# Performance work log

Hardware: AMD Instinct MI355X
Metric: run time of the kernel (lower is better)

The kernel has to match this reference:

```python
import jax, jax.numpy as jnp
import numpy as np

B, N_BOX, NUM_CLASSES = 32, 50, 20
FEATURE_SIZES = np.array([[52, 52], [26, 26], [13, 13]])
NUM_CENG = FEATURE_SIZES[:, 0] * FEATURE_SIZES[:, 1]            # [2704, 676, 169]
NUM_TOTAL = int((NUM_CENG * 3).sum())                            # 10647
ANCS_SCALE = np.array([[10, 13], [16, 30], [33, 23], [30, 61], [62, 45],
                       [59, 119], [116, 90], [156, 198], [373, 326]], dtype=np.float32) / 416.0
NEG_IOU_THRESHOLD = 0.5
NUM_NEG = 1000
EPS = 1e-7

def _build_anchor_grid():
    # rows ordered: level(52,26,13) -> cell (row-major) -> 3 anchors per cell
    out = []
    for lvl in range(3):
        f = int(FEATURE_SIZES[lvl, 0])
        ys, xs = np.meshgrid(np.arange(f), np.arange(f), indexing='ij')
        xy = (np.stack([xs, ys], -1).reshape(-1, 2).astype(np.float32)) / f  # cell corner (col/f,row/f)
        xy3 = np.repeat(xy, 3, axis=0)                                       # [f*f*3, 2]
        wh3 = np.tile(ANCS_SCALE[lvl * 3:(lvl + 1) * 3], (f * f, 1))
        out.append(np.concatenate([xy3, wh3], 1))
    return np.concatenate(out, 0)                                            # [10647, 4]

ANCS = jnp.asarray(_build_anchor_grid())
FSIZES = jnp.asarray(np.repeat(FEATURE_SIZES[:, 0].astype(np.float32), NUM_CENG * 3))  # [10647]
OFF_CENG = jnp.asarray([0.0, 2704.0, 3380.0])   # prefix sums of NUM_CENG
FW_LVL = jnp.asarray([52.0, 26.0, 13.0])


def _xywh2ltrb(xywh):
    return jnp.concatenate([xywh[..., :2] - xywh[..., 2:] * 0.5,
                            xywh[..., :2] + xywh[..., 2:] * 0.5], -1)


def _ciou(a, b):
    # a, b: broadcastable [..., 4] ltrb -> CIoU [...]
    lt = jnp.maximum(a[..., :2], b[..., :2])
    rb = jnp.minimum(a[..., 2:], b[..., 2:])
    wh = jnp.clip(rb - lt, 0.0)
    inter = wh[..., 0] * wh[..., 1]
    wa = a[..., 2] - a[..., 0]; ha = a[..., 3] - a[..., 1]
    wb = b[..., 2] - b[..., 0]; hb = b[..., 3] - b[..., 1]
    union = wa * ha + wb * hb - inter
    iou = inter / (union + EPS)
    clt = jnp.minimum(a[..., :2], b[..., :2])
    crb = jnp.maximum(a[..., 2:], b[..., 2:])
    cwh = crb - clt
    c2 = cwh[..., 0] ** 2 + cwh[..., 1] ** 2 + EPS
    ctr_a = (a[..., :2] + a[..., 2:]) * 0.5
    ctr_b = (b[..., :2] + b[..., 2:]) * 0.5
    rho2 = jnp.sum((ctr_a - ctr_b) ** 2, -1)
    v = (4.0 / (jnp.pi ** 2)) * (jnp.arctan(wa / (ha + EPS)) - jnp.arctan(wb / (hb + EPS))) ** 2
    alpha = jax.lax.stop_gradient(v / (1.0 - iou + v + EPS))
    return iou - rho2 / c2 - alpha * v


def _bce(p, t):
    p = jnp.clip(p, EPS, 1.0 - EPS)
    return -(t * jnp.log(p) + (1.0 - t) * jnp.log(1.0 - p))


def _per_image(p, boxes, labels):
    # p: [10647, 25], boxes: [N,4] ltrb, labels: [N] (1-based)
    N = boxes.shape[0]
    bxy = (boxes[:, :2] + boxes[:, 2:]) * 0.5
    bwh = boxes[:, 2:] - boxes[:, :2]
    # ---- anchor-target matching (source's loop always takes argmax anchor) ----
    p1xy = jnp.repeat(bxy, 9, axis=0)                                       # [N*9, 2]
    fpairs = jnp.repeat(jnp.asarray(FEATURE_SIZES, jnp.float32), 3, axis=0)  # [9, 2]
    p2f = jnp.tile(fpairs, (N, 1))                                          # [N*9, 2]
    colrow = jnp.floor(p1xy * p2f)                                          # (col, row) per box/anchor
    anc_xy = colrow / p2f
    anc_wh = jnp.tile(jnp.asarray(ANCS_SCALE), (N, 1))
    anc_ltrb = _xywh2ltrb(jnp.concatenate([anc_xy, anc_wh], 1))
    ids = jnp.arange(N, dtype=boxes.dtype)
    iou_m = _ciou(boxes[:, None, :] + ids[:, None, None],
                  anc_ltrb[None, :, :] + jnp.repeat(ids, 9)[None, :, None])  # [N, N*9]
    k = jnp.argmax(iou_m, axis=1) % 9                                       # best anchor id 0..8
    lvl = k // 3                                                            # (source quirk: //len(NUMS_ANC))
    cr = colrow[jnp.arange(N) * 9 + k]                                      # [N, 2]
    off_cr = cr[:, 1] * FW_LVL[lvl] + cr[:, 0]
    midx = ((OFF_CENG[lvl] + off_cr) * 3.0 + lvl.astype(jnp.float32)).astype(jnp.int32)  # [N]
    # ---- decode predictions ----
    p_box_xy = p[:, :2] / FSIZES[:, None] + ANCS[:, :2]
    p_box_wh = jnp.exp(p[:, 2:4]) * ANCS[:, 2:]
    p_ltrb = _xywh2ltrb(jnp.concatenate([p_box_xy, p_box_wh], -1))          # [10647, 4]
    # ---- positive losses ----
    pcls = p[midx, 5:]                                                      # [N, C]
    t = jax.nn.one_hot(labels - 1, NUM_CLASSES, dtype=pcls.dtype)
    l_cls = _bce(pcls, t).sum()
    pconf = p[midx, 4]
    l_conf_p = (-jnp.log(jnp.clip(pconf, EPS, 1.0 - EPS))).sum()
    ciou_pos = _ciou(boxes, p_ltrb[midx])                                   # [N]
    w = 2.0 - bwh[:, 0] * bwh[:, 1]
    l_box = (w * (1.0 - ciou_pos)).sum()
    # ---- negative conf loss (replicates filtered-coordinate indexing) ----
    iou_all = _ciou(boxes[:, None, :], p_ltrb[None, :, :])                  # [N, 10647]
    mx = iou_all.max(axis=0)
    mask = mx < NEG_IOU_THRESHOLD
    key = jnp.where(mask, mx, jnp.inf)
    order = jnp.argsort(key)                                                # masked-in first, ascending
    rank = jnp.cumsum(mask) - 1                                             # filtered coordinate per row
    neg_idx = rank[order][:NUM_NEG]                                         # == source's _max_index[:NUM_NEG]
    pneg = p[neg_idx, 4]
    l_conf_n = (-jnp.log(jnp.clip(1.0 - pneg, EPS, 1.0 - EPS))).sum()
    nf = jnp.asarray(N, p.dtype)
    return l_cls / nf, l_box / nf, l_conf_p / nf, l_conf_n


def setup_inputs() -> dict:
    key = jax.random.key(0)
    k1, k2, k3, k4 = jax.random.split(key, 4)
    p_yolo_ts = jax.random.uniform(k1, (B, NUM_TOTAL, 4 + 1 + NUM_CLASSES),
                                   dtype=jnp.float32, minval=1e-4, maxval=1.0 - 1e-4)
    cxy = jax.random.uniform(k2, (B, N_BOX, 2), minval=0.15, maxval=0.85)
    wh = jax.random.uniform(k3, (B, N_BOX, 2), minval=0.05, maxval=0.25)
    boxes = jnp.concatenate([cxy - wh * 0.5, cxy + wh * 0.5], -1).astype(jnp.float32)
    labels = jax.random.randint(k4, (B, N_BOX), 1, NUM_CLASSES + 1, dtype=jnp.int32)
    return {"p_yolo_ts": p_yolo_ts, "boxes": boxes, "labels": labels}


def reference(p_yolo_ts, boxes, labels):
    l_cls, l_box, l_cp, l_cn = jax.vmap(_per_image)(p_yolo_ts, boxes, labels)
    return l_cp.mean() + l_cn.mean() + l_box.mean() + l_cls.mean()
```

## Files before the change

kernel.cpp:

```cpp
#include <hip/hip_runtime.h>

namespace {

constexpr int BB   = 32;
constexpr int NBOX = 50;
constexpr int NCLS = 20;
constexpr int NT   = 10647;
constexpr int NNEG = 1000;
constexpr int DEC_BLOCKS = (NT + 127) / 128;
constexpr int POS_BLOCKS = (NBOX + 3) / 4;
constexpr float EPS = 1e-7f;
constexpr float PI4 = (float)(4.0 / 9.869604401089358);

__device__ __constant__ float c_aw[9] = {10.f/416.f,16.f/416.f,33.f/416.f,30.f/416.f,62.f/416.f,59.f/416.f,116.f/416.f,156.f/416.f,373.f/416.f};
__device__ __constant__ float c_ah[9] = {13.f/416.f,30.f/416.f,23.f/416.f,61.f/416.f,45.f/416.f,119.f/416.f,90.f/416.f,198.f/416.f,326.f/416.f};

__device__ __forceinline__ float fastrcp(float x) {
  return __builtin_amdgcn_rcpf(x);
}

__device__ __forceinline__ float dciou(float al, float at, float ar, float ab,
                                       float bl, float bt, float br, float bb,
                                       float atanA, float atanB) {
  float ltx = fmaxf(al, bl), lty = fmaxf(at, bt);
  float rbx = fminf(ar, br), rby = fminf(ab, bb);
  float wx = fmaxf(rbx - ltx, 0.f), wy = fmaxf(rby - lty, 0.f);
  float inter = wx * wy;
  float wa = ar - al, ha = ab - at;
  float wb = br - bl, hb = bb - bt;
  float uni = wa * ha + wb * hb - inter;
  float iou = inter / (uni + EPS);
  float cw = fmaxf(ar, br) - fminf(al, bl);
  float ch = fmaxf(ab, bb) - fminf(at, bt);
  float c2 = cw * cw + ch * ch + EPS;
  float dx = (al + ar) * 0.5f - (bl + br) * 0.5f;
  float dy = (at + ab) * 0.5f - (bt + bb) * 0.5f;
  float rho2 = dx * dx + dy * dy;
  float dat = atanA - atanB;
  float v = PI4 * (dat * dat);
  float alpha = v / (1.f - iou + v + EPS);
  return iou - rho2 / c2 - alpha * v;
}

__device__ __forceinline__ int wave_incl_scan(int x, int lane) {
  #pragma unroll
  for (int off = 1; off < 64; off <<= 1) {
    int y = __shfl_up(x, off);
    if (lane >= off) x += y;
  }
  return x;
}

__global__ __launch_bounds__(256) void k_main(const float* __restrict__ p,
                            const float* __restrict__ boxes,
                            const int* __restrict__ labels,
                            unsigned long long* __restrict__ comp,
                            float* __restrict__ pcls, float* __restrict__ pbox,
                            float* __restrict__ pcp, float* __restrict__ out) {
  const int b = blockIdx.y;
  const int tid = threadIdx.x;
  if (blockIdx.x == 0 && b == 0 && tid == 0) out[0] = 0.f;

  if (blockIdx.x < DEC_BLOCKS) {
    __shared__ float4 sA[NBOX];
    __shared__ float4 sE[NBOX];
    if (tid < NBOX) {
      const float* bp = boxes + (b * NBOX + tid) * 4;
      float l = bp[0], t = bp[1], r = bp[2], d = bp[3];
      sA[tid] = make_float4(l, t, r, d);
      float wa = r - l, ha = d - t;
      sE[tid] = make_float4((l + r) * 0.5f, (t + d) * 0.5f,
                            atanf(wa / (ha + EPS)), wa * ha);
    }
    __syncthreads();

    const int par = tid & 1;
    const int j = blockIdx.x * 128 + (tid >> 1);
    if (j >= NT) return;

    int lvl = (j < 8112) ? 0 : ((j < 10140) ? 1 : 2);
    int jb0 = (lvl == 0) ? 0 : ((lvl == 1) ? 8112 : 10140);
    int f   = (lvl == 0) ? 52 : ((lvl == 1) ? 26 : 13);
    int jj = j - jb0;
    int cell = jj / 3, a = jj % 3 + lvl * 3;
    int x = cell % f, y = cell / f;
    float ff = (float)f;
    const float* pr = p + ((size_t)b * NT + j) * 25;
    float px = pr[0] / ff + (float)x / ff;
    float py = pr[1] / ff + (float)y / ff;
    float pw = expf(pr[2]) * c_aw[a];
    float ph = expf(pr[3]) * c_ah[a];
    float bl = px - pw * 0.5f, bt = py - ph * 0.5f;
    float br = px + pw * 0.5f, bbv = py + ph * 0.5f;
    float wb = br - bl, hb = bbv - bt;
    float areab = wb * hb;
    float cxb = (bl + br) * 0.5f, cyb = (bt + bbv) * 0.5f;
    float atb = atanf(wb / (hb + EPS));

    float mx = -INFINITY;
    for (int i = par; i < NBOX; i += 2) {
      float4 A = sA[i];
      float ltx = fmaxf(A.x, bl), lty = fmaxf(A.y, bt);
      float rbx = fminf(A.z, br), rby = fminf(A.w, bbv);
      float wx = fmaxf(rbx - ltx, 0.f), wy = fmaxf(rby - lty, 0.f);
      float inter = wx * wy;
      bool need = (inter > 0.f) || (mx < 0.f);
      if (__any(need)) {
        float4 E = sE[i];
        float uni = E.w + areab - inter;
        float iou = inter * fastrcp(uni + EPS);
        float cw = fmaxf(A.z, br) - fminf(A.x, bl);
        float ch = fmaxf(A.w, bbv) - fminf(A.y, bt);
        float c2 = cw * cw + ch * ch + EPS;
        float dx = E.x - cxb;
        float dy = E.y - cyb;
        float rho2 = dx * dx + dy * dy;
        float dat = E.z - atb;
        float v = PI4 * (dat * dat);
        float alpha = v * fastrcp(1.f - iou + v + EPS);
        float ci = iou - rho2 * fastrcp(c2) - alpha * v;
        mx = fmaxf(mx, ci);
      }
    }
    mx = fmaxf(mx, __shfl_xor(mx, 1));

    if (par == 0) {
      float key = (mx < 0.5f) ? mx : INFINITY;
      unsigned int u = __float_as_uint(key);
      u = (u & 0x80000000u) ? ~u : (u | 0x80000000u);
      comp[(size_t)b * NT + j] = ((unsigned long long)u << 14) | (unsigned long long)j;
    }
  } else {
    const int lane = tid & 63;
    const int wave = tid >> 6;
    const int i = (blockIdx.x - DEC_BLOCKS) * 4 + wave;

    __shared__ float scx[NBOX], scy[NBOX];
    if (tid < NBOX) {
      const float* bp = boxes + (b * NBOX + tid) * 4;
      float l = bp[0], t = bp[1], r = bp[2], d = bp[3];
      scx[tid] = (l + r) * 0.5f;
      scy[tid] = (t + d) * 0.5f;
    }
    __syncthreads();
    if (i >= NBOX) return;

    const float* bi = boxes + (b * NBOX + i) * 4;
    float bl0 = bi[0], bt0 = bi[1], br0 = bi[2], bd0 = bi[3];
    float fi = (float)i;
    float al = bl0 + fi, at = bt0 + fi, ar = br0 + fi, ad = bd0 + fi;
    float wa = ar - al, ha = ad - at;
    float atanA = atanf(wa / (ha + EPS));

    float bestv = -INFINITY; int bestm = 1 << 30;
    #pragma unroll
    for (int m = lane; m < 9 * NBOX; m += 64) {
      int jb = m / 9, aa = m % 9;
      float fa = (aa < 3) ? 52.f : (aa < 6 ? 26.f : 13.f);
      float col = floorf(scx[jb] * fa);
      float row = floorf(scy[jb] * fa);
      float ax = col / fa, ay = row / fa;
      float aw = c_aw[aa], ah = c_ah[aa];
      float fj = (float)jb;
      float bl = (ax - aw * 0.5f) + fj;
      float bt = (ay - ah * 0.5f) + fj;
      float br = (ax + aw * 0.5f) + fj;
      float bd = (ay + ah * 0.5f) + fj;
      float wb = br - bl, hb = bd - bt;
      float atanB = atanf(wb / (hb + EPS));
      float v = dciou(al, at, ar, ad, bl, bt, br, bd, atanA, atanB);
      if (v > bestv) { bestv = v; bestm = m; }
    }
    #pragma unroll
    for (int off = 32; off > 0; off >>= 1) {
      float ov = __shfl_down(bestv, off);
      int om = __shfl_down(bestm, off);
      if (ov > bestv || (ov == bestv && om < bestm)) { bestv = ov; bestm = om; }
    }
    int bm = __shfl(bestm, 0);

    int k = bm % 9;
    int lvl = k / 3;
    float fk = (k < 3) ? 52.f : (k < 6 ? 26.f : 13.f);
    float col = floorf(scx[i] * fk);
    float row = floorf(scy[i] * fk);
    float offc = (lvl == 0) ? 0.f : (lvl == 1 ? 2704.f : 3380.f);
    int midx = (int)((offc + row * fk + col) * 3.0f + (float)lvl);

    const float* prm = p + ((size_t)b * NT + midx) * 25;
    int lab = labels[b * NBOX + i] - 1;

    float lc = 0.f;
    if (lane < NCLS) {
      float pc = prm[5 + lane];
      pc = fminf(fmaxf(pc, EPS), 1.f - EPS);
      float tt = (lane == lab) ? 1.f : 0.f;
      lc = -(tt * logf(pc) + (1.f - tt) * logf(1.f - pc));
    }
    #pragma unroll
    for (int off = 32; off > 0; off >>= 1) lc += __shfl_down(lc, off);

    if (lane == 0) {
      pcls[b * NBOX + i] = lc;
      float pc4 = prm[4];
      pc4 = fminf(fmaxf(pc4, EPS), 1.f - EPS);
      pcp[b * NBOX + i] = -logf(pc4);

      int lvl2 = (midx < 8112) ? 0 : ((midx < 10140) ? 1 : 2);
      int jb0 = (lvl2 == 0) ? 0 : ((lvl2 == 1) ? 8112 : 10140);
      int f2  = (lvl2 == 0) ? 52 : ((lvl2 == 1) ? 26 : 13);
      int jj2 = midx - jb0;
      int cell2 = jj2 / 3, a2 = jj2 % 3 + lvl2 * 3;
      int xx = cell2 % f2, yy = cell2 / f2;
      float ff2 = (float)f2;
      float px = prm[0] / ff2 + (float)xx / ff2;
      float py = prm[1] / ff2 + (float)yy / ff2;
      float pw = expf(prm[2]) * c_aw[a2];
      float ph = expf(prm[3]) * c_ah[a2];
      float pbl = px - pw * 0.5f, pbt = py - ph * 0.5f;
      float pbr = px + pw * 0.5f, pbd = py + ph * 0.5f;

      float wb = pbr - pbl, hb = pbd - pbt;
      float atanB = atanf(wb / (hb + EPS));
      float wa0 = br0 - bl0, ha0 = bd0 - bt0;
      float atanA0 = atanf(wa0 / (ha0 + EPS));
      float cp = dciou(bl0, bt0, br0, bd0, pbl, pbt, pbr, pbd, atanA0, atanB);
      float w = 2.f - wa0 * ha0;
      pbox[b * NBOX + i] = w * (1.f - cp);
    }
  }
}

__global__ __launch_bounds__(1024) void k_neg2(const unsigned long long* __restrict__ comp,
                                               const float* __restrict__ p,
                                               const float* __restrict__ pcls,
                                               const float* __restrict__ pbox,
                                               const float* __restrict__ pcp,
                                               float* __restrict__ out) {
  int b = blockIdx.x;
  const unsigned long long* c = comp + (size_t)b * NT;
  const int tid = threadIdx.x, lane = tid & 63, wave = tid >> 6;

  __shared__ int hist[4096];
  __shared__ int s_w[16];
  __shared__ unsigned long long s_pref;
  __shared__ int s_rem;
  __shared__ int s_digit;
  __shared__ int s_rem_next;
  __shared__ int s_cnt;
  __shared__ float s_facc[16];
  __shared__ float s_lcn;
  __shared__ int s_tot[11][16];
  __shared__ int s_off[11][16];

  unsigned long long v[11];
  #pragma unroll
  for (int k = 0; k < 11; ++k) {
    int j = k * 1024 + tid;
    v[k] = (j < NT) ? c[j] : ~0ull;
  }

  int wincl[11];
  #pragma unroll
  for (int k = 0; k < 11; ++k) {
    unsigned long long x = v[k];
    int flag = ((x >> 14) < 0xFF800000ull) ? 1 : 0;
    int incl = wave_incl_scan(flag, lane);
    wincl[k] = incl;
    if (lane == 63) s_tot[k][wave] = incl;
  }
  __syncthreads();
  if (wave == 0) {
    int i0 = lane * 3;
    int a0 = (i0     < 176) ? s_tot[i0 / 16][i0 % 16] : 0;
    int a1 = (i0 + 1 < 176) ? s_tot[(i0 + 1) / 16][(i0 + 1) % 16] : 0;
    int a2 = (i0 + 2 < 176) ? s_tot[(i0 + 2) / 16][(i0 + 2) % 16] : 0;
    int lsum = a0 + a1 + a2;
    int linc = wave_incl_scan(lsum, lane);
    int lexc = linc - lsum;
    if (i0     < 176) s_off[i0 / 16][i0 % 16] = lexc;
    if (i0 + 1 < 176) s_off[(i0 + 1) / 16][(i0 + 1) % 16] = lexc + a0;
    if (i0 + 2 < 176) s_off[(i0 + 2) / 16][(i0 + 2) % 16] = lexc + a0 + a1;
    if (lane == 63) s_cnt = linc;
  }
  if (tid == 0) { s_pref = 0ull; s_rem = NNEG - 1; }
  __syncthreads();
  const bool spec = (s_cnt >= NNEG);

  for (int pass = 0; pass < 4; ++pass) {
    int lo = 36 - pass * 12;
    for (int h = tid; h < 4096; h += 1024) hist[h] = 0;
    __syncthreads();
    unsigned long long pref = s_pref;
    #pragma unroll
    for (int k = 0; k < 11; ++k) {
      unsigned long long x = v[k];
      bool fin = ((x >> 14) < 0xFF800000ull);
      if ((!spec || fin) && (x >> (lo + 12)) == (pref >> (lo + 12)))
        atomicAdd(&hist[(int)((x >> lo) & 4095ull)], 1);
    }
    __syncthreads();
    int base = tid * 4;
    int c0 = hist[base], c1 = hist[base + 1], c2 = hist[base + 2], c3 = hist[base + 3];
    int tsum = c0 + c1 + c2 + c3;
    int incl = wave_incl_scan(tsum, lane);
    if (lane == 63) s_w[wave] = incl;
    __syncthreads();
    if (wave == 0) {
      int wv = (lane < 16) ? s_w[lane] : 0;
      int wincl2 = wave_incl_scan(wv, lane);
      if (lane < 16) s_w[lane] = wincl2 - wv;
    }
    __syncthreads();
    int excl = incl - tsum + s_w[wave];
    int rem = s_rem;
    int p0 = excl, p1 = p0 + c0, p2 = p1 + c1, p3 = p2 + c2;
    if (rem >= p0 && rem < p0 + c0) { s_digit = base + 0; s_rem_next = rem - p0; }
    if (rem >= p1 && rem < p1 + c1) { s_digit = base + 1; s_rem_next = rem - p1; }
    if (rem >= p2 && rem < p2 + c2) { s_digit = base + 2; s_rem_next = rem - p2; }
    if (rem >= p3 && rem < p3 + c3) { s_digit = base + 3; s_rem_next = rem - p3; }
    __syncthreads();
    if (tid == 0) {
      s_pref |= ((unsigned long long)s_digit) << lo;
      s_rem = s_rem_next;
    }
    __syncthreads();
  }
  const unsigned long long T = s_pref;

  float acc = 0.f;
  const float* pb = p + (size_t)b * NT * 25;
  #pragma unroll
  for (int k = 0; k < 11; ++k) {
    unsigned long long x = v[k];
    if (x <= T) {
      int idx = s_off[k][wave] + wincl[k] - 1;
      if (idx < 0) idx += NT;
      float q = 1.f - pb[(size_t)idx * 25 + 4];
      q = fminf(fmaxf(q, EPS), 1.f - EPS);
      acc += -logf(q);
    }
  }

  #pragma unroll
  for (int off = 32; off > 0; off >>= 1) acc += __shfl_down(acc, off);
  if (lane == 0) s_facc[wave] = acc;
  __syncthreads();
  if (tid == 0) {
    float s = 0.f;
    #pragma unroll
    for (int w = 0; w < 16; ++w) s += s_facc[w];
    s_lcn = s;
  }
  __syncthreads();

  if (wave == 0) {
    float s3 = 0.f;
    if (lane < NBOX)
      s3 = pcls[b * NBOX + lane] + pbox[b * NBOX + lane] + pcp[b * NBOX + lane];
    #pragma unroll
    for (int off = 32; off > 0; off >>= 1) s3 += __shfl_down(s3, off);
    if (lane == 0)
      atomicAdd(out, (s3 / (float)NBOX + s_lcn) / (float)BB);
  }
}

}

extern "C" void kernel_launch(void* const* d_in, const int* in_sizes, int n_in,
                              void* d_out, int out_size, void* d_ws, size_t ws_size,
                              hipStream_t stream) {
  const float* p      = (const float*)d_in[0];
  const float* boxes  = (const float*)d_in[1];
  const int*   labels = (const int*)d_in[2];
  float* out = (float*)d_out;

  char* ws = (char*)d_ws;
  size_t off = 0;
  unsigned long long* comp = (unsigned long long*)(ws + off); off += (size_t)BB * NT * sizeof(unsigned long long);
  float* pcls = (float*)(ws + off);                off += BB * NBOX * sizeof(float);
  float* pbox = (float*)(ws + off);                off += BB * NBOX * sizeof(float);
  float* pcp  = (float*)(ws + off);                off += BB * NBOX * sizeof(float);

  dim3 g1(DEC_BLOCKS + POS_BLOCKS, BB);
  k_main<<<g1, 256, 0, stream>>>(p, boxes, labels, comp, pcls, pbox, pcp, out);
  k_neg2<<<BB, 1024, 0, stream>>>(comp, p, pcls, pbox, pcp, out);
}
```

Before: 56.79 us.

## Fuse decode, positive and negative-selection kernels into one with per-image counters

```diff
diff --git a/kernel.cpp b/kernel.cpp
--- a/kernel.cpp
+++ b/kernel.cpp
@@ -7,8 +7,9 @@
 constexpr int NCLS = 20;
 constexpr int NT   = 10647;
 constexpr int NNEG = 1000;
-constexpr int DEC_BLOCKS = (NT + 127) / 128;
-constexpr int POS_BLOCKS = (NBOX + 3) / 4;
+constexpr int DECB = (NT + 511) / 512;
+constexpr int POSB = (NBOX + 15) / 16;
+constexpr int NPUB = DECB + POSB;
 constexpr float EPS = 1e-7f;
 constexpr float PI4 = (float)(4.0 / 9.869604401089358);
 
@@ -51,17 +52,18 @@
   return x;
 }
 
-__global__ __launch_bounds__(256) void k_main(const float* __restrict__ p,
+__global__ __launch_bounds__(1024) void k_all(const float* __restrict__ p,
                             const float* __restrict__ boxes,
                             const int* __restrict__ labels,
                             unsigned long long* __restrict__ comp,
                             float* __restrict__ pcls, float* __restrict__ pbox,
-                            float* __restrict__ pcp, float* __restrict__ out) {
+                            float* __restrict__ pcp, int* __restrict__ ctr,
+                            float* __restrict__ out) {
   const int b = blockIdx.y;
   const int tid = threadIdx.x;
-  if (blockIdx.x == 0 && b == 0 && tid == 0) out[0] = 0.f;
-
-  if (blockIdx.x < DEC_BLOCKS) {
+  const int lane = tid & 63, wave = tid >> 6;
+
+  if (blockIdx.x < DECB) {
     __shared__ float4 sA[NBOX];
     __shared__ float4 sE[NBOX];
     if (tid < NBOX) {
@@ -75,38 +77,36 @@
     __syncthreads();
 
     const int par = tid & 1;
-    const int j = blockIdx.x * 128 + (tid >> 1);
-    if (j >= NT) return;
-
-    int lvl = (j < 8112) ? 0 : ((j < 10140) ? 1 : 2);
-    int jb0 = (lvl == 0) ? 0 : ((lvl == 1) ? 8112 : 10140);
-    int f   = (lvl == 0) ? 52 : ((lvl == 1) ? 26 : 13);
-    int jj = j - jb0;
-    int cell = jj / 3, a = jj % 3 + lvl * 3;
-    int x = cell % f, y = cell / f;
-    float ff = (float)f;
-    const float* pr = p + ((size_t)b * NT + j) * 25;
-    float px = pr[0] / ff + (float)x / ff;
-    float py = pr[1] / ff + (float)y / ff;
-    float pw = expf(pr[2]) * c_aw[a];
-    float ph = expf(pr[3]) * c_ah[a];
-    float bl = px - pw * 0.5f, bt = py - ph * 0.5f;
-    float br = px + pw * 0.5f, bbv = py + ph * 0.5f;
-    float wb = br - bl, hb = bbv - bt;
-    float areab = wb * hb;
-    float cxb = (bl + br) * 0.5f, cyb = (bt + bbv) * 0.5f;
-    float atb = atanf(wb / (hb + EPS));
-
-    float mx = -INFINITY;
-    for (int i = par; i < NBOX; i += 2) {
-      float4 A = sA[i];
-      float ltx = fmaxf(A.x, bl), lty = fmaxf(A.y, bt);
-      float rbx = fminf(A.z, br), rby = fminf(A.w, bbv);
-      float wx = fmaxf(rbx - ltx, 0.f), wy = fmaxf(rby - lty, 0.f);
-      float inter = wx * wy;
-      bool need = (inter > 0.f) || (mx < 0.f);
-      if (__any(need)) {
+    const int j = blockIdx.x * 512 + (tid >> 1);
+    if (j < NT) {
+      int lvl = (j < 8112) ? 0 : ((j < 10140) ? 1 : 2);
+      int jb0 = (lvl == 0) ? 0 : ((lvl == 1) ? 8112 : 10140);
+      int f   = (lvl == 0) ? 52 : ((lvl == 1) ? 26 : 13);
+      int jj = j - jb0;
+      int cell = jj / 3, a = jj % 3 + lvl * 3;
+      int x = cell % f, y = cell / f;
+      float ff = (float)f;
+      const float* pr = p + ((size_t)b * NT + j) * 25;
+      float px = pr[0] / ff + (float)x / ff;
+      float py = pr[1] / ff + (float)y / ff;
+      float pw = expf(pr[2]) * c_aw[a];
+      float ph = expf(pr[3]) * c_ah[a];
+      float bl = px - pw * 0.5f, bt = py - ph * 0.5f;
+      float br = px + pw * 0.5f, bbv = py + ph * 0.5f;
+      float wb = br - bl, hb = bbv - bt;
+      float areab = wb * hb;
+      float cxb = (bl + br) * 0.5f, cyb = (bt + bbv) * 0.5f;
+      float atb = atanf(wb / (hb + EPS));
+
+      float mx = -INFINITY;
+      #pragma unroll 5
+      for (int i = par; i < NBOX; i += 2) {
+        float4 A = sA[i];
         float4 E = sE[i];
+        float ltx = fmaxf(A.x, bl), lty = fmaxf(A.y, bt);
+        float rbx = fminf(A.z, br), rby = fminf(A.w, bbv);
+        float wx = fmaxf(rbx - ltx, 0.f), wy = fmaxf(rby - lty, 0.f);
+        float inter = wx * wy;
         float uni = E.w + areab - inter;
         float iou = inter * fastrcp(uni + EPS);
         float cw = fmaxf(A.z, br) - fminf(A.x, bl);
@@ -121,19 +121,20 @@
         float ci = iou - rho2 * fastrcp(c2) - alpha * v;
         mx = fmaxf(mx, ci);
       }
-    }
-    mx = fmaxf(mx, __shfl_xor(mx, 1));
-
-    if (par == 0) {
-      float key = (mx < 0.5f) ? mx : INFINITY;
-      unsigned int u = __float_as_uint(key);
-      u = (u & 0x80000000u) ? ~u : (u | 0x80000000u);
-      comp[(size_t)b * NT + j] = ((unsigned long long)u << 14) | (unsigned long long)j;
-    }
-  } else {
-    const int lane = tid & 63;
-    const int wave = tid >> 6;
-    const int i = (blockIdx.x - DEC_BLOCKS) * 4 + wave;
+      mx = fmaxf(mx, __shfl_xor(mx, 1));
+
+      if (par == 0) {
+        float key = (mx < 0.5f) ? mx : INFINITY;
+        unsigned int u = __float_as_uint(key);
+        u = (u & 0x80000000u) ? ~u : (u | 0x80000000u);
+        comp[(size_t)b * NT + j] = ((unsigned long long)u << 14) | (unsigned long long)j;
+      }
+    }
+    __syncthreads();
+    if (tid == 0) { __threadfence(); atomicAdd(&ctr[b], 1); }
+
+  } else if (blockIdx.x < NPUB) {
+    const int i = (blockIdx.x - DECB) * 16 + wave;
 
     __shared__ float scx[NBOX], scy[NBOX];
     if (tid < NBOX) {
@@ -143,225 +144,225 @@
       scy[tid] = (t + d) * 0.5f;
     }
     __syncthreads();
-    if (i >= NBOX) return;
-
-    const float* bi = boxes + (b * NBOX + i) * 4;
-    float bl0 = bi[0], bt0 = bi[1], br0 = bi[2], bd0 = bi[3];
-    float fi = (float)i;
-    float al = bl0 + fi, at = bt0 + fi, ar = br0 + fi, ad = bd0 + fi;
-    float wa = ar - al, ha = ad - at;
-    float atanA = atanf(wa / (ha + EPS));
-
-    float bestv = -INFINITY; int bestm = 1 << 30;
+
+    if (i < NBOX) {
+      const float* bi = boxes + (b * NBOX + i) * 4;
+      float bl0 = bi[0], bt0 = bi[1], br0 = bi[2], bd0 = bi[3];
+      float fi = (float)i;
+      float al = bl0 + fi, at = bt0 + fi, ar = br0 + fi, ad = bd0 + fi;
+      float wa = ar - al, ha = ad - at;
+      float atanA = atanf(wa / (ha + EPS));
+
+      float bestv = -INFINITY; int bestm = 1 << 30;
+      #pragma unroll
+      for (int m = lane; m < 9 * NBOX; m += 64) {
+        int jb = m / 9, aa = m % 9;
+        float fa = (aa < 3) ? 52.f : (aa < 6 ? 26.f : 13.f);
+        float col = floorf(scx[jb] * fa);
+        float row = floorf(scy[jb] * fa);
+        float ax = col / fa, ay = row / fa;
+        float aw = c_aw[aa], ah = c_ah[aa];
+        float fj = (float)jb;
+        float bl = (ax - aw * 0.5f) + fj;
+        float bt = (ay - ah * 0.5f) + fj;
+        float br = (ax + aw * 0.5f) + fj;
+        float bd = (ay + ah * 0.5f) + fj;
+        float wb = br - bl, hb = bd - bt;
+        float atanB = atanf(wb / (hb + EPS));
+        float v = dciou(al, at, ar, ad, bl, bt, br, bd, atanA, atanB);
+        if (v > bestv) { bestv = v; bestm = m; }
+      }
+      #pragma unroll
+      for (int off = 32; off > 0; off >>= 1) {
+        float ov = __shfl_down(bestv, off);
+        int om = __shfl_down(bestm, off);
+        if (ov > bestv || (ov == bestv && om < bestm)) { bestv = ov; bestm = om; }
+      }
+      int bm = __shfl(bestm, 0);
+
+      int k = bm % 9;
+      int lvl = k / 3;
+      float fk = (k < 3) ? 52.f : (k < 6 ? 26.f : 13.f);
+      float col = floorf(scx[i] * fk);
+      float row = floorf(scy[i] * fk);
+      float offc = (lvl == 0) ? 0.f : (lvl == 1 ? 2704.f : 3380.f);
+      int midx = (int)((offc + row * fk + col) * 3.0f + (float)lvl);
+
+      const float* prm = p + ((size_t)b * NT + midx) * 25;
+      int lab = labels[b * NBOX + i] - 1;
+
+      float lc = 0.f;
+      if (lane < NCLS) {
+        float pc = prm[5 + lane];
+        pc = fminf(fmaxf(pc, EPS), 1.f - EPS);
+        float tt = (lane == lab) ? 1.f : 0.f;
+        lc = -(tt * logf(pc) + (1.f - tt) * logf(1.f - pc));
+      }
+      #pragma unroll
+      for (int off = 32; off > 0; off >>= 1) lc += __shfl_down(lc, off);
+
+      if (lane == 0) {
+        pcls[b * NBOX + i] = lc;
+        float pc4 = prm[4];
+        pc4 = fminf(fmaxf(pc4, EPS), 1.f - EPS);
+        pcp[b * NBOX + i] = -logf(pc4);
+
+        int lvl2 = (midx < 8112) ? 0 : ((midx < 10140) ? 1 : 2);
+        int jb0 = (lvl2 == 0) ? 0 : ((lvl2 == 1) ? 8112 : 10140);
+        int f2  = (lvl2 == 0) ? 52 : ((lvl2 == 1) ? 26 : 13);
+        int jj2 = midx - jb0;
+        int cell2 = jj2 / 3, a2 = jj2 % 3 + lvl2 * 3;
+        int xx = cell2 % f2, yy = cell2 / f2;
+        float ff2 = (float)f2;
+        float px = prm[0] / ff2 + (float)xx / ff2;
+        float py = prm[1] / ff2 + (float)yy / ff2;
+        float pw = expf(prm[2]) * c_aw[a2];
+        float ph = expf(prm[3]) * c_ah[a2];
+        float pbl = px - pw * 0.5f, pbt = py - ph * 0.5f;
+        float pbr = px + pw * 0.5f, pbd = py + ph * 0.5f;
+
+        float wb = pbr - pbl, hb = pbd - pbt;
+        float atanB = atanf(wb / (hb + EPS));
+        float wa0 = br0 - bl0, ha0 = bd0 - bt0;
+        float atanA0 = atanf(wa0 / (ha0 + EPS));
+        float cp = dciou(bl0, bt0, br0, bd0, pbl, pbt, pbr, pbd, atanA0, atanB);
+        float w = 2.f - wa0 * ha0;
+        pbox[b * NBOX + i] = w * (1.f - cp);
+      }
+    }
+    __syncthreads();
+    if (tid == 0) { __threadfence(); atomicAdd(&ctr[b], 1); }
+
+  } else {
+    if (tid == 0) {
+      while (atomicAdd(&ctr[b], 0) < NPUB) __builtin_amdgcn_s_sleep(2);
+      __threadfence();
+    }
+    __syncthreads();
+
+    const unsigned long long* c = comp + (size_t)b * NT;
+    __shared__ int hist[4096];
+    __shared__ int s_w[16];
+    __shared__ unsigned long long s_pref;
+    __shared__ int s_rem;
+    __shared__ int s_digit;
+    __shared__ int s_rem_next;
+    __shared__ int s_cnt;
+    __shared__ float s_facc[16];
+    __shared__ float s_lcn;
+    __shared__ int s_tot[11][16];
+    __shared__ int s_off[11][16];
+
+    unsigned long long v[11];
     #pragma unroll
-    for (int m = lane; m < 9 * NBOX; m += 64) {
-      int jb = m / 9, aa = m % 9;
-      float fa = (aa < 3) ? 52.f : (aa < 6 ? 26.f : 13.f);
-      float col = floorf(scx[jb] * fa);
-      float row = floorf(scy[jb] * fa);
-      float ax = col / fa, ay = row / fa;
-      float aw = c_aw[aa], ah = c_ah[aa];
-      float fj = (float)jb;
-      float bl = (ax - aw * 0.5f) + fj;
-      float bt = (ay - ah * 0.5f) + fj;
-      float br = (ax + aw * 0.5f) + fj;
-      float bd = (ay + ah * 0.5f) + fj;
-      float wb = br - bl, hb = bd - bt;
-      float atanB = atanf(wb / (hb + EPS));
-      float v = dciou(al, at, ar, ad, bl, bt, br, bd, atanA, atanB);
-      if (v > bestv) { bestv = v; bestm = m; }
-    }
-    #pragma unroll
-    for (int off = 32; off > 0; off >>= 1) {
-      float ov = __shfl_down(bestv, off);
-      int om = __shfl_down(bestm, off);
-      if (ov > bestv || (ov == bestv && om < bestm)) { bestv = ov; bestm = om; }
-    }
-    int bm = __shfl(bestm, 0);
-
-    int k = bm % 9;
-    int lvl = k / 3;
-    float fk = (k < 3) ? 52.f : (k < 6 ? 26.f : 13.f);
-    float col = floorf(scx[i] * fk);
-    float row = floorf(scy[i] * fk);
-    float offc = (lvl == 0) ? 0.f : (lvl == 1 ? 2704.f : 3380.f);
-    int midx = (int)((offc + row * fk + col) * 3.0f + (float)lvl);
-
-    const float* prm = p + ((size_t)b * NT + midx) * 25;
-    int lab = labels[b * NBOX + i] - 1;
-
-    float lc = 0.f;
-    if (lane < NCLS) {
-      float pc = prm[5 + lane];
-      pc = fminf(fmaxf(pc, EPS), 1.f - EPS);
-      float tt = (lane == lab) ? 1.f : 0.f;
-      lc = -(tt * logf(pc) + (1.f - tt) * logf(1.f - pc));
-    }
-    #pragma unroll
-    for (int off = 32; off > 0; off >>= 1) lc += __shfl_down(lc, off);
-
-    if (lane == 0) {
-      pcls[b * NBOX + i] = lc;
-      float pc4 = prm[4];
-      pc4 = fminf(fmaxf(pc4, EPS), 1.f - EPS);
-      pcp[b * NBOX + i] = -logf(pc4);
-
-      int lvl2 = (midx < 8112) ? 0 : ((midx < 10140) ? 1 : 2);
-      int jb0 = (lvl2 == 0) ? 0 : ((lvl2 == 1) ? 8112 : 10140);
-      int f2  = (lvl2 == 0) ? 52 : ((lvl2 == 1) ? 26 : 13);
-      int jj2 = midx - jb0;
-      int cell2 = jj2 / 3, a2 = jj2 % 3 + lvl2 * 3;
-      int xx = cell2 % f2, yy = cell2 / f2;
-      float ff2 = (float)f2;
-      float px = prm[0] / ff2 + (float)xx / ff2;
-      float py = prm[1] / ff2 + (float)yy / ff2;
-      float pw = expf(prm[2]) * c_aw[a2];
-      float ph = expf(prm[3]) * c_ah[a2];
-      float pbl = px - pw * 0.5f, pbt = py - ph * 0.5f;
-      float pbr = px + pw * 0.5f, pbd = py + ph * 0.5f;
-
-      float wb = pbr - pbl, hb = pbd - pbt;
-      float atanB = atanf(wb / (hb + EPS));
-      float wa0 = br0 - bl0, ha0 = bd0 - bt0;
-      float atanA0 = atanf(wa0 / (ha0 + EPS));
-      float cp = dciou(bl0, bt0, br0, bd0, pbl, pbt, pbr, pbd, atanA0, atanB);
-      float w = 2.f - wa0 * ha0;
-      pbox[b * NBOX + i] = w * (1.f - cp);
-    }
-  }
-}
-
-__global__ __launch_bounds__(1024) void k_neg2(const unsigned long long* __restrict__ comp,
-                                               const float* __restrict__ p,
-                                               const float* __restrict__ pcls,
-                                               const float* __restrict__ pbox,
-                                               const float* __restrict__ pcp,
-                                               float* __restrict__ out) {
-  int b = blockIdx.x;
-  const unsigned long long* c = comp + (size_t)b * NT;
-  const int tid = threadIdx.x, lane = tid & 63, wave = tid >> 6;
-
-  __shared__ int hist[4096];
-  __shared__ int s_w[16];
-  __shared__ unsigned long long s_pref;
-  __shared__ int s_rem;
-  __shared__ int s_digit;
-  __shared__ int s_rem_next;
-  __shared__ int s_cnt;
-  __shared__ float s_facc[16];
-  __shared__ float s_lcn;
-  __shared__ int s_tot[11][16];
-  __shared__ int s_off[11][16];
-
-  unsigned long long v[11];
-  #pragma unroll
-  for (int k = 0; k < 11; ++k) {
-    int j = k * 1024 + tid;
-    v[k] = (j < NT) ? c[j] : ~0ull;
-  }
-
-  int wincl[11];
-  #pragma unroll
-  for (int k = 0; k < 11; ++k) {
-    unsigned long long x = v[k];
-    int flag = ((x >> 14) < 0xFF800000ull) ? 1 : 0;
-    int incl = wave_incl_scan(flag, lane);
-    wincl[k] = incl;
-    if (lane == 63) s_tot[k][wave] = incl;
-  }
-  __syncthreads();
-  if (wave == 0) {
-    int i0 = lane * 3;
-    int a0 = (i0     < 176) ? s_tot[i0 / 16][i0 % 16] : 0;
-    int a1 = (i0 + 1 < 176) ? s_tot[(i0 + 1) / 16][(i0 + 1) % 16] : 0;
-    int a2 = (i0 + 2 < 176) ? s_tot[(i0 + 2) / 16][(i0 + 2) % 16] : 0;
-    int lsum = a0 + a1 + a2;
-    int linc = wave_incl_scan(lsum, lane);
-    int lexc = linc - lsum;
-    if (i0     < 176) s_off[i0 / 16][i0 % 16] = lexc;
-    if (i0 + 1 < 176) s_off[(i0 + 1) / 16][(i0 + 1) % 16] = lexc + a0;
-    if (i0 + 2 < 176) s_off[(i0 + 2) / 16][(i0 + 2) % 16] = lexc + a0 + a1;
-    if (lane == 63) s_cnt = linc;
-  }
-  if (tid == 0) { s_pref = 0ull; s_rem = NNEG - 1; }
-  __syncthreads();
-  const bool spec = (s_cnt >= NNEG);
-
-  for (int pass = 0; pass < 4; ++pass) {
-    int lo = 36 - pass * 12;
-    for (int h = tid; h < 4096; h += 1024) hist[h] = 0;
-    __syncthreads();
-    unsigned long long pref = s_pref;
+    for (int k = 0; k < 11; ++k) {
+      int j = k * 1024 + tid;
+      v[k] = (j < NT) ? c[j] : ~0ull;
+    }
+
+    int wincl[11];
     #pragma unroll
     for (int k = 0; k < 11; ++k) {
       unsigned long long x = v[k];
-      bool fin = ((x >> 14) < 0xFF800000ull);
-      if ((!spec || fin) && (x >> (lo + 12)) == (pref >> (lo + 12)))
-        atomicAdd(&hist[(int)((x >> lo) & 4095ull)], 1);
-    }
-    __syncthreads();
-    int base = tid * 4;
-    int c0 = hist[base], c1 = hist[base + 1], c2 = hist[base + 2], c3 = hist[base + 3];
-    int tsum = c0 + c1 + c2 + c3;
-    int incl = wave_incl_scan(tsum, lane);
-    if (lane == 63) s_w[wave] = incl;
+      int flag = ((x >> 14) < 0xFF800000ull) ? 1 : 0;
+      int incl = wave_incl_scan(flag, lane);
+      wincl[k] = incl;
+      if (lane == 63) s_tot[k][wave] = incl;
+    }
     __syncthreads();
     if (wave == 0) {
-      int wv = (lane < 16) ? s_w[lane] : 0;
-      int wincl2 = wave_incl_scan(wv, lane);
-      if (lane < 16) s_w[lane] = wincl2 - wv;
-    }
-    __syncthreads();
-    int excl = incl - tsum + s_w[wave];
-    int rem = s_rem;
-    int p0 = excl, p1 = p0 + c0, p2 = p1 + c1, p3 = p2 + c2;
-    if (rem >= p0 && rem < p0 + c0) { s_digit = base + 0; s_rem_next = rem - p0; }
-    if (rem >= p1 && rem < p1 + c1) { s_digit = base + 1; s_rem_next = rem - p1; }
-    if (rem >= p2 && rem < p2 + c2) { s_digit = base + 2; s_rem_next = rem - p2; }
-    if (rem >= p3 && rem < p3 + c3) { s_digit = base + 3; s_rem_next = rem - p3; }
+      int i0 = lane * 3;
+      int a0 = (i0     < 176) ? s_tot[i0 / 16][i0 % 16] : 0;
+      int a1 = (i0 + 1 < 176) ? s_tot[(i0 + 1) / 16][(i0 + 1) % 16] : 0;
+      int a2 = (i0 + 2 < 176) ? s_tot[(i0 + 2) / 16][(i0 + 2) % 16] : 0;
+      int lsum = a0 + a1 + a2;
+      int linc = wave_incl_scan(lsum, lane);
+      int lexc = linc - lsum;
+      if (i0     < 176) s_off[i0 / 16][i0 % 16] = lexc;
+      if (i0 + 1 < 176) s_off[(i0 + 1) / 16][(i0 + 1) % 16] = lexc + a0;
+      if (i0 + 2 < 176) s_off[(i0 + 2) / 16][(i0 + 2) % 16] = lexc + a0 + a1;
+      if (lane == 63) s_cnt = linc;
+    }
+    if (tid == 0) { s_pref = 0ull; s_rem = NNEG - 1; }
+    __syncthreads();
+    const bool spec = (s_cnt >= NNEG);
+
+    for (int pass = 0; pass < 4; ++pass) {
+      int lo = 36 - pass * 12;
+      for (int h = tid; h < 4096; h += 1024) hist[h] = 0;
+      __syncthreads();
+      unsigned long long pref = s_pref;
+      #pragma unroll
+      for (int k = 0; k < 11; ++k) {
+        unsigned long long x = v[k];
+        bool fin = ((x >> 14) < 0xFF800000ull);
+        if ((!spec || fin) && (x >> (lo + 12)) == (pref >> (lo + 12)))
+          atomicAdd(&hist[(int)((x >> lo) & 4095ull)], 1);
+      }
+      __syncthreads();
+      int base = tid * 4;
+      int c0 = hist[base], c1 = hist[base + 1], c2 = hist[base + 2], c3 = hist[base + 3];
+      int tsum = c0 + c1 + c2 + c3;
+      int incl = wave_incl_scan(tsum, lane);
+      if (lane == 63) s_w[wave] = incl;
+      __syncthreads();
+      if (wave == 0) {
+        int wv = (lane < 16) ? s_w[lane] : 0;
+        int wincl2 = wave_incl_scan(wv, lane);
+        if (lane < 16) s_w[lane] = wincl2 - wv;
+      }
+      __syncthreads();
+      int excl = incl - tsum + s_w[wave];
+      int rem = s_rem;
+      int p0 = excl, p1 = p0 + c0, p2 = p1 + c1, p3 = p2 + c2;
+      if (rem >= p0 && rem < p0 + c0) { s_digit = base + 0; s_rem_next = rem - p0; }
+      if (rem >= p1 && rem < p1 + c1) { s_digit = base + 1; s_rem_next = rem - p1; }
+      if (rem >= p2 && rem < p2 + c2) { s_digit = base + 2; s_rem_next = rem - p2; }
+      if (rem >= p3 && rem < p3 + c3) { s_digit = base + 3; s_rem_next = rem - p3; }
+      __syncthreads();
+      if (tid == 0) {
+        s_pref |= ((unsigned long long)s_digit) << lo;
+        s_rem = s_rem_next;
+      }
+      __syncthreads();
+    }
+    const unsigned long long T = s_pref;
+
+    float acc = 0.f;
+    const float* pb = p + (size_t)b * NT * 25;
+    #pragma unroll
+    for (int k = 0; k < 11; ++k) {
+      unsigned long long x = v[k];
+      if (x <= T) {
+        int idx = s_off[k][wave] + wincl[k] - 1;
+        if (idx < 0) idx += NT;
+        float q = 1.f - pb[(size_t)idx * 25 + 4];
+        q = fminf(fmaxf(q, EPS), 1.f - EPS);
+        acc += -logf(q);
+      }
+    }
+
+    #pragma unroll
+    for (int off = 32; off > 0; off >>= 1) acc += __shfl_down(acc, off);
+    if (lane == 0) s_facc[wave] = acc;
     __syncthreads();
     if (tid == 0) {
-      s_pref |= ((unsigned long long)s_digit) << lo;
-      s_rem = s_rem_next;
-    }
-    __syncthreads();
-  }
-  const unsigned long long T = s_pref;
-
-  float acc = 0.f;
-  const float* pb = p + (size_t)b * NT * 25;
-  #pragma unroll
-  for (int k = 0; k < 11; ++k) {
-    unsigned long long x = v[k];
-    if (x <= T) {
-      int idx = s_off[k][wave] + wincl[k] - 1;
-      if (idx < 0) idx += NT;
-      float q = 1.f - pb[(size_t)idx * 25 + 4];
-      q = fminf(fmaxf(q, EPS), 1.f - EPS);
-      acc += -logf(q);
-    }
-  }
-
-  #pragma unroll
-  for (int off = 32; off > 0; off >>= 1) acc += __shfl_down(acc, off);
-  if (lane == 0) s_facc[wave] = acc;
-  __syncthreads();
-  if (tid == 0) {
-    float s = 0.f;
-    #pragma unroll
-    for (int w = 0; w < 16; ++w) s += s_facc[w];
-    s_lcn = s;
-  }
-  __syncthreads();
-
-  if (wave == 0) {
-    float s3 = 0.f;
-    if (lane < NBOX)
-      s3 = pcls[b * NBOX + lane] + pbox[b * NBOX + lane] + pcp[b * NBOX + lane];
-    #pragma unroll
-    for (int off = 32; off > 0; off >>= 1) s3 += __shfl_down(s3, off);
-    if (lane == 0)
-      atomicAdd(out, (s3 / (float)NBOX + s_lcn) / (float)BB);
+      float s = 0.f;
+      #pragma unroll
+      for (int w = 0; w < 16; ++w) s += s_facc[w];
+      s_lcn = s;
+    }
+    __syncthreads();
+
+    if (wave == 0) {
+      float s3 = 0.f;
+      if (lane < NBOX)
+        s3 = pcls[b * NBOX + lane] + pbox[b * NBOX + lane] + pcp[b * NBOX + lane];
+      #pragma unroll
+      for (int off = 32; off > 0; off >>= 1) s3 += __shfl_down(s3, off);
+      if (lane == 0)
+        atomicAdd(out, (s3 / (float)NBOX + s_lcn) / (float)BB);
+    }
   }
 }
 
@@ -381,8 +382,10 @@
   float* pcls = (float*)(ws + off);                off += BB * NBOX * sizeof(float);
   float* pbox = (float*)(ws + off);                off += BB * NBOX * sizeof(float);
   float* pcp  = (float*)(ws + off);                off += BB * NBOX * sizeof(float);
-
-  dim3 g1(DEC_BLOCKS + POS_BLOCKS, BB);
-  k_main<<<g1, 256, 0, stream>>>(p, boxes, labels, comp, pcls, pbox, pcp, out);
-  k_neg2<<<BB, 1024, 0, stream>>>(comp, p, pcls, pbox, pcp, out);
-}
+  int*   ctr  = (int*)(ws + off);                  off += BB * sizeof(int);
+
+  hipMemsetAsync(ctr, 0, BB * sizeof(int), stream);
+  hipMemsetAsync(out, 0, sizeof(float), stream);
+  k_all<<<dim3(NPUB + 1, BB), 1024, 0, stream>>>(p, boxes, labels, comp,
+                                                 pcls, pbox, pcp, ctr, out);
+}
```

Measured after the change: 88.54 us. 55.9% more time.
